# Performance work log

Hardware: AMD Instinct MI355X
Metric: run time of the kernel (lower is better)

## Reference

```python
import jax, jax.numpy as jnp
from jax import lax
import numpy as np

EPS = 1e-5
NEG_SLOPE = 0.2

# 4D conv via lax.conv_general_dilated (supports arbitrary spatial rank)
_DN = ('NCABXY', 'OIABXY', 'NCABXY')  # N,C + 4 spatial dims

def conv4d(x, w):
    # x: (N, Cin, S1, S2, H, W); w: (Cout, Cin, 3, 3, 3, 3); padding=1, stride=1
    return lax.conv_general_dilated(
        x, w,
        window_strides=(1, 1, 1, 1),
        padding=[(1, 1)] * 4,
        dimension_numbers=_DN,
    )

def instance_norm4d(x):
    # normalize per (n, c) over all 4 spatial dims; no affine (PyTorch default)
    mean = jnp.mean(x, axis=(2, 3, 4, 5), keepdims=True)
    var = jnp.var(x, axis=(2, 3, 4, 5), keepdims=True)
    return (x - mean) * lax.rsqrt(var + EPS)

def leaky_relu(x):
    return jnp.where(x >= 0, x, NEG_SLOPE * x)

def setup_inputs() -> dict:
    key = jax.random.key(0)
    k0, k1, k2 = jax.random.split(key, 3)
    image = jax.random.normal(k0, (1, 16, 8, 16, 64, 64), dtype=jnp.float32)
    # He-ish init scale for kernel 3^4
    w1 = jax.random.normal(k1, (32, 16, 3, 3, 3, 3), dtype=jnp.float32) * 0.03
    w2 = jax.random.normal(k2, (32, 32, 3, 3, 3, 3), dtype=jnp.float32) * 0.02
    return {"image": image, "w1": w1, "w2": w2}

def reference(image, w1, w2):
    x = leaky_relu(instance_norm4d(conv4d(image, w1)))
    x = leaky_relu(instance_norm4d(conv4d(x, w2)))
    return x
```

## Files before the change

kernel.cpp:

```cpp
#include <hip/hip_runtime.h>

#define D1 8
#define D2 16
#define HH 64
#define WW 64
#define SPATIAL (D1*D2*HH*WW)
#define EPS 1e-5f
#define NEG 0.2f

typedef unsigned short u16;
typedef __attribute__((ext_vector_type(8))) short s16x8;
typedef __attribute__((ext_vector_type(8))) unsigned short u16x8;
typedef __attribute__((ext_vector_type(4))) unsigned short u16x4;
typedef __attribute__((ext_vector_type(4))) float f32x4;

__device__ __forceinline__ u16 f2bf(float f) {
    unsigned int u = __builtin_bit_cast(unsigned int, f);
    return (u16)((u + 0x7FFFu + ((u >> 16) & 1u)) >> 16);
}
__device__ __forceinline__ float bf2f(u16 u) {
    unsigned int v = ((unsigned int)u) << 16;
    return __builtin_bit_cast(float, v);
}
__device__ __forceinline__ float leaky(float x) {
    return x >= 0.f ? x : NEG * x;
}

__device__ __forceinline__ void decode_block(int flat, int& a, int& b, int& h0) {
    int xcd  = flat & 7;
    int slot = flat >> 3;
    int ht   = slot & 7;
    int b0   = (slot >> 3) & 1;
    a        = (slot >> 4) & 7;
    b        = xcd * 2 + b0;
    h0       = ht * 8;
}

__global__ __launch_bounds__(256) void wtrans1(const float* __restrict__ w,
                                               u16* __restrict__ o) {
    int i = blockIdx.x * 256 + threadIdx.x;
    if (i >= 55296) return;
    int k    = i & 31;
    int co   = (i >> 5) & 31;
    int grp  = (i >> 10) & 1;
    int rest = i >> 11;
    int dh   = rest % 3;
    int p    = rest / 3;
    int da = p / 3, db = p % 3;
    float v = 0.f;
    if (grp == 0) {
        int dw = k >> 4, ci = k & 15;
        v = w[((((co * 16 + ci) * 3 + da) * 3 + db) * 3 + dh) * 3 + dw];
    } else if (k < 16) {
        v = w[((((co * 16 + k) * 3 + da) * 3 + db) * 3 + dh) * 3 + 2];
    }
    o[i] = f2bf(v);
}

__global__ __launch_bounds__(256) void wtrans2(const float* __restrict__ w,
                                               u16* __restrict__ o) {
    int i = blockIdx.x * 256 + threadIdx.x;
    if (i >= 82944) return;
    int ci = i & 31;
    int co = (i >> 5) & 31;
    int t  = (i >> 10) % 9;
    int p  = (i >> 10) / 9;
    int da = p / 3, db = p % 3, dh = t / 3, dw = t % 3;
    o[i] = f2bf(w[((((co * 32 + ci) * 3 + da) * 3 + db) * 3 + dh) * 3 + dw]);
}

__global__ __launch_bounds__(256) void imgtrans(const float* __restrict__ img,
                                                u16* __restrict__ o) {
    int p = blockIdx.x * 256 + threadIdx.x;
    u16 r[16];
    #pragma unroll
    for (int c = 0; c < 16; ++c)
        r[c] = f2bf(img[(size_t)c * SPATIAL + p]);
    u16x8 lo, hi;
    #pragma unroll
    for (int j = 0; j < 8; ++j) { lo[j] = r[j]; hi[j] = r[8 + j]; }
    u16x8* dst = (u16x8*)(o + (size_t)p * 16);
    dst[0] = lo;
    dst[1] = hi;
}

__global__ __launch_bounds__(256, 2)
void conv1_mfma(const u16* __restrict__ xT, const u16* __restrict__ w1t,
                u16* __restrict__ y1, float* __restrict__ st1)
{
    __shared__ __align__(16) u16 lds[660 * 24];
    __shared__ float sred[64];

    const int tid = threadIdx.x;
    int a, b, h0;
    decode_block(blockIdx.x, a, b, h0);
    const int lane = tid & 63;
    const int wv   = tid >> 6;
    const int kq   = lane >> 4;
    const int m    = lane & 15;
    const int wseg = wv << 4;

    unsigned pm = 0;
    #pragma unroll
    for (int p = 0; p < 9; ++p) {
        int ap = a + p / 3 - 1, bp = b + p % 3 - 1;
        if (ap >= 0 && ap < D1 && bp >= 0 && bp < D2) pm |= 1u << p;
    }

    const int p0 = tid >> 1, g = tid & 1;
    unsigned vmask = 0;
    int goff[6];
    #pragma unroll
    for (int k = 0; k < 6; ++k) {
        int pos = p0 + 128 * k;
        int row = pos / 66, col = pos - row * 66;
        int h = h0 - 1 + row, w = col - 1;
        bool v = (pos < 660) && col >= 1 && col <= 64 && h >= 0 && h < HH;
        goff[k] = v ? (h * WW + w) * 16 + g * 8 : 0;
        vmask |= (unsigned)v << k;
    }
    const int lbase = p0 * 24 + g * 8;

    for (int e = tid; e < 660; e += 256) {
        int row = e / 66, col = e - row * 66;
        int h = h0 - 1 + row;
        if (col == 0 || col == 65 || h < 0 || h >= HH) {
            u16x8 z = (u16x8)0;
            *(u16x8*)&lds[e * 24]     = z;
            *(u16x8*)&lds[e * 24 + 8] = z;
        }
    }

    f32x4 acc[8][2];
    #pragma unroll
    for (int i = 0; i < 8; ++i)
        #pragma unroll
        for (int nt = 0; nt < 2; ++nt)
            acc[i][nt] = (f32x4)0.f;

    int p = 0;
    while (!((pm >> p) & 1)) ++p;

    u16x8 pf[6];
    {
        int ap = a + p / 3 - 1, bp = b + p % 3 - 1;
        const u16* src = xT + (size_t)(ap * D2 + bp) * (HH * WW * 16);
        #pragma unroll
        for (int k = 0; k < 6; ++k)
            if ((vmask >> k) & 1) pf[k] = *(const u16x8*)(src + goff[k]);
    }

    while (p < 9) {
        int pn = p + 1;
        while (pn < 9 && !((pm >> pn) & 1)) ++pn;

        #pragma unroll
        for (int k = 0; k < 6; ++k)
            if ((vmask >> k) & 1) *(u16x8*)&lds[lbase + k * 3072] = pf[k];
        __syncthreads();

        if (pn < 9) {
            int ap = a + pn / 3 - 1, bp = b + pn % 3 - 1;
            const u16* src = xT + (size_t)(ap * D2 + bp) * (HH * WW * 16);
            #pragma unroll
            for (int k = 0; k < 6; ++k)
                if ((vmask >> k) & 1) pf[k] = *(const u16x8*)(src + goff[k]);
        }

        const u16* wbase = w1t + p * 6144;
        #pragma unroll
        for (int grp = 0; grp < 2; ++grp) {
            s16x8 bf[3][2];
            #pragma unroll
            for (int dh = 0; dh < 3; ++dh) {
                const u16* wb = wbase + (dh * 2 + grp) * 1024;
                bf[dh][0] = *(const s16x8*)(wb + m * 32 + kq * 8);
                bf[dh][1] = *(const s16x8*)(wb + (m + 16) * 32 + kq * 8);
            }
            const int cshift = (grp == 0) ? (kq >> 1) : 2;
            const int ebase  = (kq & 1) * 8;
            #pragma unroll
            for (int x = 0; x < 10; ++x) {
                int pos = x * 66 + wseg + m + cshift;
                s16x8 af = *(const s16x8*)&lds[pos * 24 + ebase];
                #pragma unroll
                for (int dh = 0; dh < 3; ++dh) {
                    int i = x - dh;
                    if (i >= 0 && i < 8) {
                        acc[i][0] = __builtin_amdgcn_mfma_f32_16x16x32_bf16(af, bf[dh][0], acc[i][0], 0, 0, 0);
                        acc[i][1] = __builtin_amdgcn_mfma_f32_16x16x32_bf16(af, bf[dh][1], acc[i][1], 0, 0, 0);
                    }
                }
            }
        }
        __syncthreads();
        p = pn;
    }

    if (tid < 64) sred[tid] = 0.f;
    __syncthreads();

    float s[2] = {0.f, 0.f}, s2[2] = {0.f, 0.f};
    const size_t plane_out = (size_t)(a * D2 + b) * (HH * WW);
    #pragma unroll
    for (int i = 0; i < 8; ++i) {
        int h  = h0 + i;
        int w0 = wseg + kq * 4;
        #pragma unroll
        for (int nt = 0; nt < 2; ++nt) {
            int co = m + nt * 16;
            #pragma unroll
            for (int reg = 0; reg < 4; ++reg) {
                float v = acc[i][nt][reg];
                s[nt]  += v;
                s2[nt] += v * v;
                y1[(plane_out + h * WW + (w0 + reg)) * 32 + co] = f2bf(v);
            }
        }
    }
    #pragma unroll
    for (int nt = 0; nt < 2; ++nt) {
        s[nt]  += __shfl_xor(s[nt], 16);  s[nt]  += __shfl_xor(s[nt], 32);
        s2[nt] += __shfl_xor(s2[nt], 16); s2[nt] += __shfl_xor(s2[nt], 32);
    }
    if (kq == 0) {
        atomicAdd(&sred[m * 2],            s[0]);
        atomicAdd(&sred[m * 2 + 1],        s2[0]);
        atomicAdd(&sred[(m + 16) * 2],     s[1]);
        atomicAdd(&sred[(m + 16) * 2 + 1], s2[1]);
    }
    __syncthreads();
    if (tid < 64) atomicAdd(&st1[tid], sred[tid]);
}

__global__ __launch_bounds__(256)
void norm1_kernel(u16* __restrict__ y1, const float* __restrict__ st1)
{
    const int tid = threadIdx.x;
    const int q   = tid & 3;
    const float invN = 1.f / (float)SPATIAL;
    float mean[8], scl[8];
    #pragma unroll
    for (int j = 0; j < 8; ++j) {
        int ci  = q * 8 + j;
        float mu = st1[ci * 2] * invN;
        float va = st1[ci * 2 + 1] * invN - mu * mu;
        mean[j] = mu;
        scl[j]  = rsqrtf(va + EPS);
    }
    #pragma unroll
    for (int j4 = 0; j4 < 4; ++j4) {
        size_t gidx = (size_t)blockIdx.x * 1024 + j4 * 256 + tid;
        u16x8* ptr = (u16x8*)(y1 + gidx * 8);
        u16x8 v = *ptr;
        u16x8 o;
        #pragma unroll
        for (int j = 0; j < 8; ++j)
            o[j] = f2bf(leaky((bf2f(v[j]) - mean[j]) * scl[j]));
        *ptr = o;
    }
}

__global__ __launch_bounds__(256, 2)
void conv2_mfma(const u16* __restrict__ y1, const u16* __restrict__ w2t,
                u16* __restrict__ y2, float* __restrict__ st2)
{
    __shared__ __align__(16) u16 lds[660 * 40];
    __shared__ float sred[64];

    const int tid = threadIdx.x;
    int a, b, h0;
    decode_block(blockIdx.x, a, b, h0);
    const int lane = tid & 63;
    const int wv   = tid >> 6;
    const int kq   = lane >> 4;
    const int m    = lane & 15;
    const int wseg = wv << 4;

    unsigned pm = 0;
    #pragma unroll
    for (int p = 0; p < 9; ++p) {
        int ap = a + p / 3 - 1, bp = b + p % 3 - 1;
        if (ap >= 0 && ap < D1 && bp >= 0 && bp < D2) pm |= 1u << p;
    }

    const int p0 = tid >> 2, q = tid & 3;
    unsigned vmask = 0;
    int goff[11];
    #pragma unroll
    for (int k = 0; k < 11; ++k) {
        int pos = p0 + 64 * k;
        int row = pos / 66, col = pos - row * 66;
        int h = h0 - 1 + row, w = col - 1;
        bool v = (pos < 660) && col >= 1 && col <= 64 && h >= 0 && h < HH;
        goff[k] = v ? (h * WW + w) * 32 + q * 8 : 0;
        vmask |= (unsigned)v << k;
    }
    const int lbase = p0 * 40 + q * 8;

    for (int e = tid; e < 660; e += 256) {
        int row = e / 66, col = e - row * 66;
        int h = h0 - 1 + row;
        if (col == 0 || col == 65 || h < 0 || h >= HH) {
            u16x8 z = (u16x8)0;
            #pragma unroll
            for (int gg = 0; gg < 4; ++gg)
                *(u16x8*)&lds[e * 40 + gg * 8] = z;
        }
    }

    f32x4 acc[8][2];
    #pragma unroll
    for (int i = 0; i < 8; ++i)
        #pragma unroll
        for (int nt = 0; nt < 2; ++nt)
            acc[i][nt] = (f32x4)0.f;

    int p = 0;
    while (!((pm >> p) & 1)) ++p;

    u16x8 pf[11];
    {
        int ap = a + p / 3 - 1, bp = b + p % 3 - 1;
        const u16* src = y1 + (size_t)(ap * D2 + bp) * (HH * WW * 32);
        #pragma unroll
        for (int k = 0; k < 11; ++k)
            if ((vmask >> k) & 1) pf[k] = *(const u16x8*)(src + goff[k]);
    }

    while (p < 9) {
        int pn = p + 1;
        while (pn < 9 && !((pm >> pn) & 1)) ++pn;

        #pragma unroll
        for (int k = 0; k < 11; ++k)
            if ((vmask >> k) & 1) *(u16x8*)&lds[lbase + k * 2560] = pf[k];
        __syncthreads();

        if (pn < 9) {
            int ap = a + pn / 3 - 1, bp = b + pn % 3 - 1;
            const u16* src = y1 + (size_t)(ap * D2 + bp) * (HH * WW * 32);
            #pragma unroll
            for (int k = 0; k < 11; ++k)
                if ((vmask >> k) & 1) pf[k] = *(const u16x8*)(src + goff[k]);
        }

        const u16* wbase = w2t + p * 9216;
        #pragma unroll
        for (int dw = 0; dw < 3; ++dw) {
            s16x8 bf[3][2];
            #pragma unroll
            for (int dh = 0; dh < 3; ++dh) {
                const u16* wb = wbase + (dh * 3 + dw) * 1024;
                bf[dh][0] = *(const s16x8*)(wb + m * 32 + kq * 8);
                bf[dh][1] = *(const s16x8*)(wb + (m + 16) * 32 + kq * 8);
            }
            #pragma unroll
            for (int x = 0; x < 10; ++x) {
                int pos = x * 66 + wseg + dw + m;
                s16x8 af = *(const s16x8*)&lds[pos * 40 + kq * 8];
                #pragma unroll
                for (int dh = 0; dh < 3; ++dh) {
                    int i = x - dh;
                    if (i >= 0 && i < 8) {
                        acc[i][0] = __builtin_amdgcn_mfma_f32_16x16x32_bf16(af, bf[dh][0], acc[i][0], 0, 0, 0);
                        acc[i][1] = __builtin_amdgcn_mfma_f32_16x16x32_bf16(af, bf[dh][1], acc[i][1], 0, 0, 0);
                    }
                }
            }
        }
        __syncthreads();
        p = pn;
    }

    if (tid < 64) sred[tid] = 0.f;
    __syncthreads();

    float s[2] = {0.f, 0.f}, s2[2] = {0.f, 0.f};
    #pragma unroll
    for (int i = 0; i < 8; ++i) {
        int h  = h0 + i;
        int w0 = wseg + kq * 4;
        #pragma unroll
        for (int nt = 0; nt < 2; ++nt) {
            int co = m + nt * 16;
            u16x4 pk;
            #pragma unroll
            for (int reg = 0; reg < 4; ++reg) {
                float v = acc[i][nt][reg];
                s[nt]  += v;
                s2[nt] += v * v;
                pk[reg] = f2bf(v);
            }
            size_t off = ((size_t)(co * D1 + a) * D2 + b) * (HH * WW) + h * WW + w0;
            *(u16x4*)(y2 + off) = pk;
        }
    }
    #pragma unroll
    for (int nt = 0; nt < 2; ++nt) {
        s[nt]  += __shfl_xor(s[nt], 16);  s[nt]  += __shfl_xor(s[nt], 32);
        s2[nt] += __shfl_xor(s2[nt], 16); s2[nt] += __shfl_xor(s2[nt], 32);
    }
    if (kq == 0) {
        atomicAdd(&sred[m * 2],            s[0]);
        atomicAdd(&sred[m * 2 + 1],        s2[0]);
        atomicAdd(&sred[(m + 16) * 2],     s[1]);
        atomicAdd(&sred[(m + 16) * 2 + 1], s2[1]);
    }
    __syncthreads();
    if (tid < 64) atomicAdd(&st2[tid], sred[tid]);
}

__global__ __launch_bounds__(256)
void norm2_kernel(const u16* __restrict__ y2, const float* __restrict__ st2,
                  float* __restrict__ out)
{
    size_t i4 = (size_t)blockIdx.x * 256 + threadIdx.x;
    int c = (int)(i4 >> 17);
    const float invN = 1.f / (float)SPATIAL;
    float mu = st2[c * 2] * invN;
    float va = st2[c * 2 + 1] * invN - mu * mu;
    float sc = rsqrtf(va + EPS);
    u16x4 v = *(const u16x4*)(y2 + i4 * 4);
    float4 o;
    o.x = leaky((bf2f(v[0]) - mu) * sc);
    o.y = leaky((bf2f(v[1]) - mu) * sc);
    o.z = leaky((bf2f(v[2]) - mu) * sc);
    o.w = leaky((bf2f(v[3]) - mu) * sc);
    *(float4*)(out + i4 * 4) = o;
}

extern "C" void kernel_launch(void* const* d_in, const int* in_sizes, int n_in,
                              void* d_out, int out_size, void* d_ws, size_t ws_size,
                              hipStream_t stream)
{
    const float* image = (const float*)d_in[0];
    const float* w1    = (const float*)d_in[1];
    const float* w2    = (const float*)d_in[2];
    float* out = (float*)d_out;

    u16*   imgT = (u16*)d_ws;
    u16*   y1   = (u16*)((char*)d_ws + 33554432);
    u16*   y2   = imgT;
    float* st   = (float*)((char*)d_ws + 67108864);
    float* st1  = st;
    float* st2  = st + 64;

    u16* w1t = (u16*)((char*)d_out + 66832384);
    u16* w2t = (u16*)((char*)d_out + 66942976);

    hipMemsetAsync(st, 0, 512, stream);
    wtrans1<<<216, 256, 0, stream>>>(w1, w1t);
    wtrans2<<<324, 256, 0, stream>>>(w2, w2t);
    imgtrans<<<2048, 256, 0, stream>>>(image, imgT);

    conv1_mfma<<<1024, 256, 0, stream>>>(imgT, w1t, y1, st1);
    norm1_kernel<<<2048, 256, 0, stream>>>(y1, st1);
    conv2_mfma<<<1024, 256, 0, stream>>>(y1, w2t, y2, st2);
    norm2_kernel<<<16384, 256, 0, stream>>>(y2, st2, out);
}
```

Baseline: 277.2 us.

## Use zero-padded global layouts and read conv operands directly, dropping LDS staging

The image and intermediate activations are stored in zero-padded layouts, with halos on every spatial dim, that are memset each call. Both conv kernels then drop the LDS staging, barriers and boundary masking and load MFMA A-fragments straight from global memory through L1/L2. Occupancy hints rise to 3 blocks per SM. This removes the LDS store and sync overhead but adds two large memsets and relies on cache hits for repeated global loads of the same halo data.

```diff
diff --git a/kernel.cpp b/kernel.cpp
--- a/kernel.cpp
+++ b/kernel.cpp
@@ -7,6 +7,17 @@
 #define SPATIAL (D1*D2*HH*WW)
 #define EPS 1e-5f
 #define NEG 0.2f
+
+#define PA 10
+#define PB 18
+#define PH 66
+#define PW 66
+#define IT_H 1056
+#define IT_P 69696
+#define IT_A 1254528
+#define Y1_H 2112
+#define Y1_P 139392
+#define Y1_A 2509056
 
 typedef unsigned short u16;
 typedef __attribute__((ext_vector_type(8))) short s16x8;
@@ -72,6 +83,7 @@
 __global__ __launch_bounds__(256) void imgtrans(const float* __restrict__ img,
                                                 u16* __restrict__ o) {
     int p = blockIdx.x * 256 + threadIdx.x;
+    int a = p >> 16, b = (p >> 12) & 15, h = (p >> 6) & 63, w = p & 63;
     u16 r[16];
     #pragma unroll
     for (int c = 0; c < 16; ++c)
@@ -79,18 +91,18 @@
     u16x8 lo, hi;
     #pragma unroll
     for (int j = 0; j < 8; ++j) { lo[j] = r[j]; hi[j] = r[8 + j]; }
-    u16x8* dst = (u16x8*)(o + (size_t)p * 16);
+    size_t off = (size_t)(a + 1) * IT_A + (size_t)(b + 1) * IT_P
+               + (h + 1) * IT_H + (w + 1) * 16;
+    u16x8* dst = (u16x8*)(o + off);
     dst[0] = lo;
     dst[1] = hi;
 }
 
-__global__ __launch_bounds__(256, 2)
-void conv1_mfma(const u16* __restrict__ xT, const u16* __restrict__ w1t,
-                u16* __restrict__ y1, float* __restrict__ st1)
-{
-    __shared__ __align__(16) u16 lds[660 * 24];
+__global__ __launch_bounds__(256, 3)
+void conv1_mfma(const u16* __restrict__ xTp, const u16* __restrict__ w1t,
+                u16* __restrict__ y1p, float* __restrict__ st1)
+{
     __shared__ float sred[64];
-
     const int tid = threadIdx.x;
     int a, b, h0;
     decode_block(blockIdx.x, a, b, h0);
@@ -107,30 +119,6 @@
         if (ap >= 0 && ap < D1 && bp >= 0 && bp < D2) pm |= 1u << p;
     }
 
-    const int p0 = tid >> 1, g = tid & 1;
-    unsigned vmask = 0;
-    int goff[6];
-    #pragma unroll
-    for (int k = 0; k < 6; ++k) {
-        int pos = p0 + 128 * k;
-        int row = pos / 66, col = pos - row * 66;
-        int h = h0 - 1 + row, w = col - 1;
-        bool v = (pos < 660) && col >= 1 && col <= 64 && h >= 0 && h < HH;
-        goff[k] = v ? (h * WW + w) * 16 + g * 8 : 0;
-        vmask |= (unsigned)v << k;
-    }
-    const int lbase = p0 * 24 + g * 8;
-
-    for (int e = tid; e < 660; e += 256) {
-        int row = e / 66, col = e - row * 66;
-        int h = h0 - 1 + row;
-        if (col == 0 || col == 65 || h < 0 || h >= HH) {
-            u16x8 z = (u16x8)0;
-            *(u16x8*)&lds[e * 24]     = z;
-            *(u16x8*)&lds[e * 24 + 8] = z;
-        }
-    }
-
     f32x4 acc[8][2];
     #pragma unroll
     for (int i = 0; i < 8; ++i)
@@ -138,74 +126,53 @@
         for (int nt = 0; nt < 2; ++nt)
             acc[i][nt] = (f32x4)0.f;
 
-    int p = 0;
-    while (!((pm >> p) & 1)) ++p;
-
-    u16x8 pf[6];
-    {
-        int ap = a + p / 3 - 1, bp = b + p % 3 - 1;
-        const u16* src = xT + (size_t)(ap * D2 + bp) * (HH * WW * 16);
-        #pragma unroll
-        for (int k = 0; k < 6; ++k)
-            if ((vmask >> k) & 1) pf[k] = *(const u16x8*)(src + goff[k]);
-    }
-
-    while (p < 9) {
-        int pn = p + 1;
-        while (pn < 9 && !((pm >> pn) & 1)) ++pn;
-
-        #pragma unroll
-        for (int k = 0; k < 6; ++k)
-            if ((vmask >> k) & 1) *(u16x8*)&lds[lbase + k * 3072] = pf[k];
-        __syncthreads();
-
-        if (pn < 9) {
-            int ap = a + pn / 3 - 1, bp = b + pn % 3 - 1;
-            const u16* src = xT + (size_t)(ap * D2 + bp) * (HH * WW * 16);
-            #pragma unroll
-            for (int k = 0; k < 6; ++k)
-                if ((vmask >> k) & 1) pf[k] = *(const u16x8*)(src + goff[k]);
+    const int aoff0 = (wseg + (kq >> 1) + m) * 16 + (kq & 1) * 8;
+    const int aoff1 = (wseg + 2 + m) * 16 + (kq & 1) * 8;
+
+    for (int p = 0; p < 9; ++p) {
+        if (!((pm >> p) & 1)) continue;
+        const int da = p / 3, db = p % 3;
+        const u16* rowp = xTp + (size_t)(a + da) * IT_A + (size_t)(b + db) * IT_P
+                        + h0 * IT_H;
+        const u16* wb = w1t + p * 6144;
+
+        s16x8 bf[3][2][2];
+        #pragma unroll
+        for (int dh = 0; dh < 3; ++dh)
+            #pragma unroll
+            for (int grp = 0; grp < 2; ++grp) {
+                const u16* wg = wb + (dh * 2 + grp) * 1024;
+                bf[dh][grp][0] = *(const s16x8*)(wg + m * 32 + kq * 8);
+                bf[dh][grp][1] = *(const s16x8*)(wg + (m + 16) * 32 + kq * 8);
+            }
+
+        #pragma unroll
+        for (int x = 0; x < 10; ++x) {
+            const u16* rp = rowp + x * IT_H;
+            s16x8 a0 = *(const s16x8*)(rp + aoff0);
+            s16x8 a1 = *(const s16x8*)(rp + aoff1);
+            #pragma unroll
+            for (int dh = 0; dh < 3; ++dh) {
+                int i = x - dh;
+                if (i >= 0 && i < 8) {
+                    acc[i][0] = __builtin_amdgcn_mfma_f32_16x16x32_bf16(a0, bf[dh][0][0], acc[i][0], 0, 0, 0);
+                    acc[i][1] = __builtin_amdgcn_mfma_f32_16x16x32_bf16(a0, bf[dh][0][1], acc[i][1], 0, 0, 0);
+                    acc[i][0] = __builtin_amdgcn_mfma_f32_16x16x32_bf16(a1, bf[dh][1][0], acc[i][0], 0, 0, 0);
+                    acc[i][1] = __builtin_amdgcn_mfma_f32_16x16x32_bf16(a1, bf[dh][1][1], acc[i][1], 0, 0, 0);
+                }
+            }
         }
-
-        const u16* wbase = w1t + p * 6144;
-        #pragma unroll
-        for (int grp = 0; grp < 2; ++grp) {
-            s16x8 bf[3][2];
-            #pragma unroll
-            for (int dh = 0; dh < 3; ++dh) {
-                const u16* wb = wbase + (dh * 2 + grp) * 1024;
-                bf[dh][0] = *(const s16x8*)(wb + m * 32 + kq * 8);
-                bf[dh][1] = *(const s16x8*)(wb + (m + 16) * 32 + kq * 8);
-            }
-            const int cshift = (grp == 0) ? (kq >> 1) : 2;
-            const int ebase  = (kq & 1) * 8;
-            #pragma unroll
-            for (int x = 0; x < 10; ++x) {
-                int pos = x * 66 + wseg + m + cshift;
-                s16x8 af = *(const s16x8*)&lds[pos * 24 + ebase];
-                #pragma unroll
-                for (int dh = 0; dh < 3; ++dh) {
-                    int i = x - dh;
-                    if (i >= 0 && i < 8) {
-                        acc[i][0] = __builtin_amdgcn_mfma_f32_16x16x32_bf16(af, bf[dh][0], acc[i][0], 0, 0, 0);
-                        acc[i][1] = __builtin_amdgcn_mfma_f32_16x16x32_bf16(af, bf[dh][1], acc[i][1], 0, 0, 0);
-                    }
-                }
-            }
-        }
-        __syncthreads();
-        p = pn;
     }
 
     if (tid < 64) sred[tid] = 0.f;
     __syncthreads();
 
     float s[2] = {0.f, 0.f}, s2[2] = {0.f, 0.f};
-    const size_t plane_out = (size_t)(a * D2 + b) * (HH * WW);
+    const size_t ob = (size_t)(a + 1) * Y1_A + (size_t)(b + 1) * Y1_P;
     #pragma unroll
     for (int i = 0; i < 8; ++i) {
-        int h  = h0 + i;
-        int w0 = wseg + kq * 4;
+        int h = h0 + i + 1;
+        int w0 = wseg + kq * 4 + 1;
         #pragma unroll
         for (int nt = 0; nt < 2; ++nt) {
             int co = m + nt * 16;
@@ -214,7 +181,7 @@
                 float v = acc[i][nt][reg];
                 s[nt]  += v;
                 s2[nt] += v * v;
-                y1[(plane_out + h * WW + (w0 + reg)) * 32 + co] = f2bf(v);
+                y1p[ob + h * Y1_H + (w0 + reg) * 32 + co] = f2bf(v);
             }
         }
     }
@@ -234,9 +201,13 @@
 }
 
 __global__ __launch_bounds__(256)
-void norm1_kernel(u16* __restrict__ y1, const float* __restrict__ st1)
+void norm1_kernel(u16* __restrict__ y1p, const float* __restrict__ st1)
 {
     const int tid = threadIdx.x;
+    const int r   = blockIdx.x;
+    const int a   = r >> 10;
+    const int b   = (r >> 6) & 15;
+    const int h   = r & 63;
     const int q   = tid & 3;
     const float invN = 1.f / (float)SPATIAL;
     float mean[8], scl[8];
@@ -248,26 +219,22 @@
         mean[j] = mu;
         scl[j]  = rsqrtf(va + EPS);
     }
-    #pragma unroll
-    for (int j4 = 0; j4 < 4; ++j4) {
-        size_t gidx = (size_t)blockIdx.x * 1024 + j4 * 256 + tid;
-        u16x8* ptr = (u16x8*)(y1 + gidx * 8);
-        u16x8 v = *ptr;
-        u16x8 o;
-        #pragma unroll
-        for (int j = 0; j < 8; ++j)
-            o[j] = f2bf(leaky((bf2f(v[j]) - mean[j]) * scl[j]));
-        *ptr = o;
-    }
-}
-
-__global__ __launch_bounds__(256, 2)
-void conv2_mfma(const u16* __restrict__ y1, const u16* __restrict__ w2t,
+    size_t base = (size_t)(a + 1) * Y1_A + (size_t)(b + 1) * Y1_P
+                + (h + 1) * Y1_H + 32;
+    u16x8* ptr = (u16x8*)(y1p + base) + tid;
+    u16x8 v = *ptr;
+    u16x8 o;
+    #pragma unroll
+    for (int j = 0; j < 8; ++j)
+        o[j] = f2bf(leaky((bf2f(v[j]) - mean[j]) * scl[j]));
+    *ptr = o;
+}
+
+__global__ __launch_bounds__(256, 3)
+void conv2_mfma(const u16* __restrict__ y1p, const u16* __restrict__ w2t,
                 u16* __restrict__ y2, float* __restrict__ st2)
 {
-    __shared__ __align__(16) u16 lds[660 * 40];
     __shared__ float sred[64];
-
     const int tid = threadIdx.x;
     int a, b, h0;
     decode_block(blockIdx.x, a, b, h0);
@@ -284,31 +251,6 @@
         if (ap >= 0 && ap < D1 && bp >= 0 && bp < D2) pm |= 1u << p;
     }
 
-    const int p0 = tid >> 2, q = tid & 3;
-    unsigned vmask = 0;
-    int goff[11];
-    #pragma unroll
-    for (int k = 0; k < 11; ++k) {
-        int pos = p0 + 64 * k;
-        int row = pos / 66, col = pos - row * 66;
-        int h = h0 - 1 + row, w = col - 1;
-        bool v = (pos < 660) && col >= 1 && col <= 64 && h >= 0 && h < HH;
-        goff[k] = v ? (h * WW + w) * 32 + q * 8 : 0;
-        vmask |= (unsigned)v << k;
-    }
-    const int lbase = p0 * 40 + q * 8;
-
-    for (int e = tid; e < 660; e += 256) {
-        int row = e / 66, col = e - row * 66;
-        int h = h0 - 1 + row;
-        if (col == 0 || col == 65 || h < 0 || h >= HH) {
-            u16x8 z = (u16x8)0;
-            #pragma unroll
-            for (int gg = 0; gg < 4; ++gg)
-                *(u16x8*)&lds[e * 40 + gg * 8] = z;
-        }
-    }
-
     f32x4 acc[8][2];
     #pragma unroll
     for (int i = 0; i < 8; ++i)
@@ -316,61 +258,44 @@
         for (int nt = 0; nt < 2; ++nt)
             acc[i][nt] = (f32x4)0.f;
 
-    int p = 0;
-    while (!((pm >> p) & 1)) ++p;
-
-    u16x8 pf[11];
-    {
-        int ap = a + p / 3 - 1, bp = b + p % 3 - 1;
-        const u16* src = y1 + (size_t)(ap * D2 + bp) * (HH * WW * 32);
-        #pragma unroll
-        for (int k = 0; k < 11; ++k)
-            if ((vmask >> k) & 1) pf[k] = *(const u16x8*)(src + goff[k]);
-    }
-
-    while (p < 9) {
-        int pn = p + 1;
-        while (pn < 9 && !((pm >> pn) & 1)) ++pn;
-
-        #pragma unroll
-        for (int k = 0; k < 11; ++k)
-            if ((vmask >> k) & 1) *(u16x8*)&lds[lbase + k * 2560] = pf[k];
-        __syncthreads();
-
-        if (pn < 9) {
-            int ap = a + pn / 3 - 1, bp = b + pn % 3 - 1;
-            const u16* src = y1 + (size_t)(ap * D2 + bp) * (HH * WW * 32);
-            #pragma unroll
-            for (int k = 0; k < 11; ++k)
-                if ((vmask >> k) & 1) pf[k] = *(const u16x8*)(src + goff[k]);
+    const int aoff = (wseg + m) * 32 + kq * 8;
+
+    for (int p = 0; p < 9; ++p) {
+        if (!((pm >> p) & 1)) continue;
+        const int da = p / 3, db = p % 3;
+        const u16* rowp = y1p + (size_t)(a + da) * Y1_A + (size_t)(b + db) * Y1_P
+                        + h0 * Y1_H;
+        const u16* wb = w2t + p * 9216;
+
+        s16x8 bf[3][3][2];
+        #pragma unroll
+        for (int dh = 0; dh < 3; ++dh)
+            #pragma unroll
+            for (int dw = 0; dw < 3; ++dw) {
+                const u16* wg = wb + (dh * 3 + dw) * 1024;
+                bf[dh][dw][0] = *(const s16x8*)(wg + m * 32 + kq * 8);
+                bf[dh][dw][1] = *(const s16x8*)(wg + (m + 16) * 32 + kq * 8);
+            }
+
+        #pragma unroll
+        for (int x = 0; x < 10; ++x) {
+            const u16* rp = rowp + x * Y1_H + aoff;
+            s16x8 a0 = *(const s16x8*)(rp);
+            s16x8 a1 = *(const s16x8*)(rp + 32);
+            s16x8 a2 = *(const s16x8*)(rp + 64);
+            #pragma unroll
+            for (int dh = 0; dh < 3; ++dh) {
+                int i = x - dh;
+                if (i >= 0 && i < 8) {
+                    acc[i][0] = __builtin_amdgcn_mfma_f32_16x16x32_bf16(a0, bf[dh][0][0], acc[i][0], 0, 0, 0);
+                    acc[i][1] = __builtin_amdgcn_mfma_f32_16x16x32_bf16(a0, bf[dh][0][1], acc[i][1], 0, 0, 0);
+                    acc[i][0] = __builtin_amdgcn_mfma_f32_16x16x32_bf16(a1, bf[dh][1][0], acc[i][0], 0, 0, 0);
+                    acc[i][1] = __builtin_amdgcn_mfma_f32_16x16x32_bf16(a1, bf[dh][1][1], acc[i][1], 0, 0, 0);
+                    acc[i][0] = __builtin_amdgcn_mfma_f32_16x16x32_bf16(a2, bf[dh][2][0], acc[i][0], 0, 0, 0);
+                    acc[i][1] = __builtin_amdgcn_mfma_f32_16x16x32_bf16(a2, bf[dh][2][1], acc[i][1], 0, 0, 0);
+                }
+            }
         }
-
-        const u16* wbase = w2t + p * 9216;
-        #pragma unroll
-        for (int dw = 0; dw < 3; ++dw) {
-            s16x8 bf[3][2];
-            #pragma unroll
-            for (int dh = 0; dh < 3; ++dh) {
-                const u16* wb = wbase + (dh * 3 + dw) * 1024;
-                bf[dh][0] = *(const s16x8*)(wb + m * 32 + kq * 8);
-                bf[dh][1] = *(const s16x8*)(wb + (m + 16) * 32 + kq * 8);
-            }
-            #pragma unroll
-            for (int x = 0; x < 10; ++x) {
-                int pos = x * 66 + wseg + dw + m;
-                s16x8 af = *(const s16x8*)&lds[pos * 40 + kq * 8];
-                #pragma unroll
-                for (int dh = 0; dh < 3; ++dh) {
-                    int i = x - dh;
-                    if (i >= 0 && i < 8) {
-                        acc[i][0] = __builtin_amdgcn_mfma_f32_16x16x32_bf16(af, bf[dh][0], acc[i][0], 0, 0, 0);
-                        acc[i][1] = __builtin_amdgcn_mfma_f32_16x16x32_bf16(af, bf[dh][1], acc[i][1], 0, 0, 0);
-                    }
-                }
-            }
-        }
-        __syncthreads();
-        p = pn;
     }
 
     if (tid < 64) sred[tid] = 0.f;
@@ -439,23 +364,26 @@
     const float* w2    = (const float*)d_in[2];
     float* out = (float*)d_out;
 
-    u16*   imgT = (u16*)d_ws;
-    u16*   y1   = (u16*)((char*)d_ws + 33554432);
-    u16*   y2   = imgT;
-    float* st   = (float*)((char*)d_ws + 67108864);
-    float* st1  = st;
-    float* st2  = st + 64;
-
-    u16* w1t = (u16*)((char*)d_out + 66832384);
-    u16* w2t = (u16*)((char*)d_out + 66942976);
-
-    hipMemsetAsync(st, 0, 512, stream);
+    u16* y1p = (u16*)d_out;
+    u16* w1t = (u16*)((char*)d_out + 50331648);
+    u16* w2t = (u16*)((char*)d_out + 50442240);
+
+    u16*   imgTp = (u16*)d_ws;
+    u16*   y2    = (u16*)((char*)d_ws + 25165824);
+    float* st    = (float*)((char*)d_ws + 67108864);
+    float* st1   = st;
+    float* st2   = st + 64;
+
+    hipMemsetAsync(y1p,   0, 50181120, stream);
+    hipMemsetAsync(imgTp, 0, 25090560, stream);
+    hipMemsetAsync(st,    0, 512,      stream);
+
     wtrans1<<<216, 256, 0, stream>>>(w1, w1t);
     wtrans2<<<324, 256, 0, stream>>>(w2, w2t);
-    imgtrans<<<2048, 256, 0, stream>>>(image, imgT);
-
-    conv1_mfma<<<1024, 256, 0, stream>>>(imgT, w1t, y1, st1);
-    norm1_kernel<<<2048, 256, 0, stream>>>(y1, st1);
-    conv2_mfma<<<1024, 256, 0, stream>>>(y1, w2t, y2, st2);
+    imgtrans<<<2048, 256, 0, stream>>>(image, imgTp);
+
+    conv1_mfma<<<1024, 256, 0, stream>>>(imgTp, w1t, y1p, st1);
+    norm1_kernel<<<8192, 256, 0, stream>>>(y1p, st1);
+    conv2_mfma<<<1024, 256, 0, stream>>>(y1p, w2t, y2, st2);
     norm2_kernel<<<16384, 256, 0, stream>>>(y2, st2, out);
 }
```

Result: slower. 330.3 us (+19.1%).
